# Performance work log

Measured on AMD Instinct MI355X. Metric: run time of the kernel, lower is better.

The kernel has to match this reference:

```python
import jax, jax.numpy as jnp
import numpy as np
import math

D_MODEL = 1024
NUM_HEADS = 16
ALPHA, BETA, K_SCALE, C_THRESHOLD = 0.7, 0.3, 5.0, 0.3
TAU_SCHEDULE = [0.05, 0.05, 0.05, 0.15, 0.25, 0.35, 0.45, 0.55, 0.65, 0.7, 0.75, 0.8]


def setup_inputs() -> dict:
    key = jax.random.key(0)
    ks = jax.random.split(key, 6)
    B, S = 2, 1024
    scale = D_MODEL ** -0.5
    return {
        "x": jax.random.normal(ks[0], (B, S, D_MODEL), dtype=jnp.float32),
        "entropy_prev": jax.random.uniform(ks[1], (B, NUM_HEADS, S, 1), dtype=jnp.float32),
        "Wq": jax.random.normal(ks[2], (D_MODEL, D_MODEL), dtype=jnp.float32) * scale,
        "Wk": jax.random.normal(ks[3], (D_MODEL, D_MODEL), dtype=jnp.float32) * scale,
        "Wv": jax.random.normal(ks[4], (D_MODEL, D_MODEL), dtype=jnp.float32) * scale,
        "Wo": jax.random.normal(ks[5], (D_MODEL, D_MODEL), dtype=jnp.float32) * scale,
        "layer_idx": 4,
    }


def _proj(x, W, B, S, H, Dh):
    # nn.Linear(bias=False): y = x @ W.T ; then [B,S,H,Dh] -> [B,H,S,Dh]
    return jnp.einsum('bsd,ed->bse', x, W).reshape(B, S, H, Dh).transpose(0, 2, 1, 3)


def reference(x, entropy_prev, Wq, Wk, Wv, Wo, layer_idx):
    B, S, _ = x.shape
    H = NUM_HEADS
    Dh = D_MODEL // H
    tau = TAU_SCHEDULE[int(layer_idx)]

    Q = _proj(x, Wq, B, S, H, Dh)
    K = _proj(x, Wk, B, S, H, Dh)
    V = _proj(x, Wv, B, S, H, Dh)

    # raw scores [B,H,S,S]
    scores_raw = jnp.einsum('bhqd,bhkd->bhqk', Q, K) / math.sqrt(Dh)

    # key salience [B,H,1,S]
    sal = jnp.minimum((K * K).sum(axis=-1) / float(Dh), 2.0)
    sal_b = sal[:, :, None, :]

    # WIPER gate [B,H,S,S] (entropy_prev broadcasts over key dim)
    E_t = jax.nn.sigmoid(K_SCALE * (entropy_prev - C_THRESHOLD))
    gate_logit = jnp.clip(E_t * 5.0 + ALPHA * sal_b * 2.0 - BETA * entropy_prev * 1.0, -20.0, 20.0)
    gate = jax.nn.sigmoid(gate_logit)

    mask = gate >= tau
    scores_gated = jnp.where(mask, scores_raw + jnp.log(gate + 1e-8), -jnp.inf)

    best_k_idx = jnp.argmax(scores_raw, axis=-1)  # [B,H,S]
    any_finite = mask.any(axis=-1, keepdims=True)  # [B,H,S,1]

    # safe softmax: degenerate (all -inf) rows replaced by 0s, result discarded below
    attn_raw = jax.nn.softmax(jnp.where(any_finite, scores_gated, 0.0), axis=-1)
    keep_one = jax.nn.one_hot(best_k_idx, S, dtype=x.dtype)
    attn = jnp.where(any_finite, attn_raw, keep_one)

    O = jnp.einsum('bhqk,bhkd->bhqd', attn, V)

    # entropy state: S = log(l) - E[s']
    max_scores = scores_gated.max(axis=-1, keepdims=True)
    shifted = scores_gated - max_scores
    fm = jnp.isfinite(shifted)
    shifted_safe = jnp.where(fm, shifted, 0.0)
    exp_scores = jnp.where(fm, jnp.exp(shifted_safe), 0.0)
    l = jnp.maximum(exp_scores.sum(axis=-1, keepdims=True), 1e-20)
    weighted = (exp_scores * shifted_safe).sum(axis=-1, keepdims=True)
    S_state = jnp.where(any_finite, jnp.log(l) - weighted / l, 0.0)

    out = jnp.einsum('bsd,ed->bse', O.transpose(0, 2, 1, 3).reshape(B, S, D_MODEL), Wo)
    return out, S_state
```

## Files before the change

### kernel.cpp

```cpp
#include <hip/hip_runtime.h>
#include <hip/hip_cooperative_groups.h>
#include <cstdint>

namespace cg = cooperative_groups;

#define DEVINL __device__ __forceinline__

typedef __attribute__((ext_vector_type(8))) short bf16x8;
typedef __attribute__((ext_vector_type(4))) float f32x4;
typedef __attribute__((ext_vector_type(8))) unsigned short u16x8;
typedef unsigned short u16;
typedef unsigned int u32;

#define MFMA16(a, b, c) __builtin_amdgcn_mfma_f32_16x16x32_bf16(a, b, c, 0, 0, 0)

#define LOG2E 1.4426950408889634f
#define LN2 0.69314718055994531f

DEVINL u16 f2bf(float x) {
  u32 u = __builtin_bit_cast(u32, x);
  u += 0x7FFFu + ((u >> 16) & 1u);
  return (u16)(u >> 16);
}
DEVINL float exp2fast(float x) {
  float r;
  asm("v_exp_f32 %0, %1" : "=v"(r) : "v"(x));
  return r;
}
DEVINL void gload_lds16(const void* g, void* l) {
  __builtin_amdgcn_global_load_lds(
      (const __attribute__((address_space(1))) unsigned int*)g,
      (__attribute__((address_space(3))) unsigned int*)l, 16, 0, 0);
}

static constexpr size_t OFF_XB = 0;
static constexpr size_t OFF_WB = 4ull << 20;
static constexpr size_t OFF_Q = 10ull << 20;
static constexpr size_t OFF_K = 14ull << 20;
static constexpr size_t OFF_OB = 18ull << 20;
static constexpr size_t OFF_VT = 22ull << 20;
static constexpr size_t OFF_WOB = 26ull << 20;
static constexpr size_t OFF_FQ = 28ull << 20;
static constexpr size_t OFF_GK = (28ull << 20) + (128ull << 10);

__global__ __launch_bounds__(256, 2) void k_mega(
    const float* __restrict__ x, const float* __restrict__ Wq,
    const float* __restrict__ Wk, const float* __restrict__ Wv,
    const float* __restrict__ Wo, const float* __restrict__ ent,
    char* __restrict__ ws, float* __restrict__ outp) {
  __shared__ __align__(16) char SMEM[81920];
  u16* xb  = (u16*)(ws + OFF_XB);
  u16* Wb  = (u16*)(ws + OFF_WB);
  u16* Qb  = (u16*)(ws + OFF_Q);
  u16* Kb  = (u16*)(ws + OFF_K);
  u16* Ob  = (u16*)(ws + OFF_OB);
  u16* Vtb = (u16*)(ws + OFF_VT);
  u16* Wob = (u16*)(ws + OFF_WOB);
  float* efq = (float*)(ws + OFF_FQ);
  float* egk = (float*)(ws + OFF_GK);
  float* Sst = outp + 2097152;

  cg::grid_group grid = cg::this_grid();
  const int bid = blockIdx.x;
  const int t = threadIdx.x;
  const int lane = t & 63, w = t >> 6;
  const int lm = lane & 15, lg = lane >> 4;

  {
    const int tid = bid * 256 + t;
    for (int g = tid; g < 786432; g += 131072) {
      const float* src; u16* dst; int base;
      if (g < 262144) { src = x; dst = xb; base = g; }
      else {
        int r = (g - 262144) >> 17;
        base = (g - 262144) & 131071;
        src = r == 0 ? Wq : r == 1 ? Wk : r == 2 ? Wv : Wo;
        dst = r == 0 ? Wb : r == 1 ? Wb + 1048576 : r == 2 ? Wb + 2097152 : Wob;
      }
      const float4* s4 = (const float4*)src;
      float4 a = s4[2 * base], b2 = s4[2 * base + 1];
      u16x8 o;
      o[0] = f2bf(a.x);  o[1] = f2bf(a.y);  o[2] = f2bf(a.z);  o[3] = f2bf(a.w);
      o[4] = f2bf(b2.x); o[5] = f2bf(b2.y); o[6] = f2bf(b2.z); o[7] = f2bf(b2.w);
      *(u16x8*)(dst + 8 * base) = o;
    }
    if (bid * 256 + t < 32768) {
      int i = bid * 256 + t;
      float e = ent[i];
      float Et = 1.f / (1.f + __expf(-5.f * (e - 0.3f)));
      efq[i] = __expf(-(5.f * Et - 0.3f * e));
    }
  }
  grid.sync();

  {
    const int wr = w >> 1, wc = w & 1;
    const int rs = t >> 3, cs = t & 7;
    for (int tt = bid; tt < 768; tt += 512) {
      const int m0 = (tt & 31) * 64, n0 = (tt >> 5) * 128;
      f32x4 acc[2][4] = {};
      auto gstage = [&](int buf, int kt) {
        u16* As_ = (u16*)SMEM + buf * 12288;
        u16* Bs_ = As_ + 4096;
#pragma unroll
        for (int i = 0; i < 2; ++i) {
          int rr = rs + 32 * i;
          gload_lds16(xb + (size_t)(m0 + rr) * 1024 + kt + ((cs ^ (rr & 7)) * 8),
                      (char*)As_ + t * 16 + i * 4096);
        }
#pragma unroll
        for (int i = 0; i < 4; ++i) {
          int rr = rs + 32 * i;
          gload_lds16(Wb + (size_t)(n0 + rr) * 1024 + kt + ((cs ^ (rr & 7)) * 8),
                      (char*)Bs_ + t * 16 + i * 4096);
        }
      };
      gstage(0, 0);
      __syncthreads();
      for (int ki = 0; ki < 16; ++ki) {
        const int cur = ki & 1;
        if (ki + 1 < 16) gstage(cur ^ 1, (ki + 1) * 64);
        const u16* As = (u16*)SMEM + cur * 12288;
        const u16* Bs = As + 4096;
#pragma unroll
        for (int ks = 0; ks < 2; ++ks) {
          bf16x8 af[2], bfr[4];
#pragma unroll
          for (int mt = 0; mt < 2; ++mt) {
            int row = wr * 32 + mt * 16 + lm;
            af[mt] = *(const bf16x8*)((const char*)As + row * 128 +
                                      (((ks * 4 + lg) ^ (row & 7)) << 4));
          }
#pragma unroll
          for (int nt = 0; nt < 4; ++nt) {
            int row = wc * 64 + nt * 16 + lm;
            bfr[nt] = *(const bf16x8*)((const char*)Bs + row * 128 +
                                       (((ks * 4 + lg) ^ (row & 7)) << 4));
          }
#pragma unroll
          for (int mt = 0; mt < 2; ++mt)
#pragma unroll
            for (int nt = 0; nt < 4; ++nt)
              acc[mt][nt] = MFMA16(af[mt], bfr[nt], acc[mt][nt]);
        }
        __syncthreads();
      }
      const int region = n0 >> 10;
      const int b = m0 >> 10, s0 = m0 & 1023;
      if (region < 2) {
        u16* dst = region == 0 ? Qb : Kb;
        const float scl = region == 0 ? 0.125f * LOG2E : 1.f;
#pragma unroll
        for (int mt = 0; mt < 2; ++mt)
#pragma unroll
          for (int nt = 0; nt < 4; ++nt)
#pragma unroll
            for (int r = 0; r < 4; ++r) {
              int m = m0 + wr * 32 + mt * 16 + lg * 4 + r;
              int n = n0 + wc * 64 + nt * 16 + lm;
              int e = n & 1023, h = e >> 6, d = e & 63;
              dst[(size_t)(((b << 4) + h) * 1024 + (m & 1023)) * 64 + d] =
                  f2bf(acc[mt][nt][r] * scl);
            }
        if (region == 1) {
          int hh = ((n0 - 1024) >> 6) + wc;
#pragma unroll
          for (int mt = 0; mt < 2; ++mt)
#pragma unroll
            for (int r = 0; r < 4; ++r) {
              float ss = 0.f;
#pragma unroll
              for (int nt = 0; nt < 4; ++nt) ss += acc[mt][nt][r] * acc[mt][nt][r];
              ss += __shfl_xor(ss, 1);
              ss += __shfl_xor(ss, 2);
              ss += __shfl_xor(ss, 4);
              ss += __shfl_xor(ss, 8);
              if (lm == 0) {
                int s = s0 + wr * 32 + mt * 16 + lg * 4 + r;
                float g = 1.4f * fminf(ss * (1.f / 64.f), 2.f);
                egk[(size_t)((b << 4) + hh) * 1024 + s] = __expf(-g);
              }
            }
        }
      } else {
        u16* tile = (u16*)SMEM;
#pragma unroll
        for (int half = 0; half < 2; ++half) {
          if (wc == half) {
#pragma unroll
            for (int mt = 0; mt < 2; ++mt)
#pragma unroll
              for (int nt = 0; nt < 4; ++nt)
#pragma unroll
                for (int r = 0; r < 4; ++r) {
                  int d = nt * 16 + lm;
                  int mloc = wr * 32 + mt * 16 + lg * 4 + r;
                  tile[d * 64 + (mloc ^ ((d & 7) << 3))] = f2bf(acc[mt][nt][r]);
                }
          }
          __syncthreads();
          int hh = ((n0 - 2048) >> 6) + half;
#pragma unroll
          for (int j = 0; j < 2; ++j) {
            int dd = (t >> 3) + 32 * j, mc = t & 7;
            u16x8 v = *(const u16x8*)&tile[dd * 64 + ((mc * 8) ^ ((dd & 7) << 3))];
            *(u16x8*)(Vtb + ((size_t)(((b << 4) + hh) * 64 + dd)) * 1024 + s0 +
                      mc * 8) = v;
          }
          __syncthreads();
        }
      }
    }
  }
  grid.sync();

  {
    const int bh = bid >> 4, qblk = bid & 15;
    const int b = bh >> 4, h = bh & 15;
    const size_t bhS = (size_t)bh << 10;
    const int qb = qblk * 64 + w * 16;
    u16* KsA = (u16*)SMEM;
    u16* VsA = (u16*)(SMEM + 32768);
    u32* PsA = (u32*)(SMEM + 65536);

    auto stage = [&](int buf, int k0) {
      int rowK = t >> 3, cK = t & 7;
      int rowV = t >> 4, cV = t & 15;
#pragma unroll
      for (int i2 = 0; i2 < 4; ++i2) {
        int rr = rowK + 32 * i2;
        gload_lds16(Kb + (bhS + k0 + rr) * 64 + ((cK ^ (rr & 7)) * 8),
                    (char*)(KsA + buf * 8192) + t * 16 + i2 * 4096);
        int dd2 = rowV + 16 * i2;
        gload_lds16(Vtb + ((size_t)bh * 64 + dd2) * 1024 + k0 + ((cV ^ (dd2 & 15)) * 8),
                    (char*)(VsA + buf * 8192) + t * 16 + i2 * 4096);
      }
    };

    bf16x8 qf[2];
#pragma unroll
    for (int ks = 0; ks < 2; ++ks)
      qf[ks] = *(const bf16x8*)(Qb + (bhS + qb + lm) * 64 + ks * 32 + lg * 8);
    const float efql = efq[bhS + qb + lm];

    f32x4 Oacc[4] = {};
    float m_r = -1e30f, l_r = 0.f, W_r = 0.f;

    stage(0, 0);
    f32x4 egN[8];
#pragma unroll
    for (int nt = 0; nt < 8; ++nt)
      egN[nt] = *(const f32x4*)&egk[bhS + nt * 16 + lg * 4];
    __syncthreads();

    for (int kt = 0; kt < 8; ++kt) {
      const int cur = kt & 1;
      if (kt < 7) stage(cur ^ 1, (kt + 1) * 128);

      f32x4 c_[8];
      __builtin_amdgcn_s_setprio(1);
#pragma unroll
      for (int nt = 0; nt < 8; ++nt) {
        c_[nt] = (f32x4){0.f, 0.f, 0.f, 0.f};
#pragma unroll
        for (int ks = 0; ks < 2; ++ks) {
          int row = nt * 16 + lm;
          int byo = (((ks * 4 + lg) ^ (row & 7)) << 4);
          bf16x8 kb = *(const bf16x8*)((const char*)(KsA + cur * 8192) + row * 128 + byo);
          c_[nt] = MFMA16(kb, qf[ks], c_[nt]);
        }
      }
      __builtin_amdgcn_s_setprio(0);

      float v_[8][4];
      float lmax = -3e38f;
#pragma unroll
      for (int nt = 0; nt < 8; ++nt) {
        f32x4 eg = egN[nt];
#pragma unroll
        for (int r = 0; r < 4; ++r) {
          float xg = efql * eg[r];
          v_[nt][r] = c_[nt][r] - __log2f(1.f + xg);
        }
        lmax = fmaxf(fmaxf(lmax, v_[nt][0]),
                     fmaxf(fmaxf(v_[nt][1], v_[nt][2]), v_[nt][3]));
      }
      if (kt < 7) {
#pragma unroll
        for (int nt = 0; nt < 8; ++nt)
          egN[nt] = *(const f32x4*)&egk[bhS + (kt + 1) * 128 + nt * 16 + lg * 4];
      }
      lmax = fmaxf(lmax, __shfl_xor(lmax, 16));
      lmax = fmaxf(lmax, __shfl_xor(lmax, 32));

      if (__any(lmax > m_r + 7.2134752f)) {
        float mn = fmaxf(m_r, lmax);
        float dd = m_r - mn;
        float sc = exp2fast(dd);
        W_r = sc * (W_r + dd * l_r);
        l_r *= sc;
        m_r = mn;
        float scO[4];
#pragma unroll
        for (int r = 0; r < 4; ++r) scO[r] = __shfl(sc, (lane & 48) | (lg * 4 + r));
#pragma unroll
        for (int dt = 0; dt < 4; ++dt)
#pragma unroll
          for (int r = 0; r < 4; ++r) Oacc[dt][r] *= scO[r];
      }

      float psum = 0.f, wsum = 0.f;
      u32 pw[16];
#pragma unroll
      for (int nt = 0; nt < 8; ++nt) {
        float p_[4];
#pragma unroll
        for (int r = 0; r < 4; ++r) {
          float sh = v_[nt][r] - m_r;
          float p = exp2fast(sh);
          p_[r] = p;
          psum += p;
          wsum = fmaf(p, sh, wsum);
        }
        asm("v_cvt_pk_bf16_f32 %0, %1, %2" : "=v"(pw[nt*2+0]) : "v"(p_[0]), "v"(p_[1]));
        asm("v_cvt_pk_bf16_f32 %0, %1, %2" : "=v"(pw[nt*2+1]) : "v"(p_[2]), "v"(p_[3]));
      }
      psum += __shfl_xor(psum, 16);
      psum += __shfl_xor(psum, 32);
      wsum += __shfl_xor(wsum, 16);
      wsum += __shfl_xor(wsum, 32);
      l_r += psum;
      W_r += wsum;

      u32* prow = PsA + (w * 16 + lm) * 64;
      const int sw = (lm & 7) << 2;
#pragma unroll
      for (int nt = 0; nt < 8; ++nt) {
        int idx = (nt * 8 + lg * 2) ^ sw;
        uint2 pr;
        pr.x = pw[nt * 2 + 0];
        pr.y = pw[nt * 2 + 1];
        *(uint2*)(prow + idx) = pr;
      }

      bf16x8 pa[4];
#pragma unroll
      for (int ks = 0; ks < 4; ++ks) {
        int idx = (ks * 16 + lg * 4) ^ sw;
        pa[ks] = *(const bf16x8*)(prow + idx);
      }
      __builtin_amdgcn_s_setprio(1);
#pragma unroll
      for (int dt = 0; dt < 4; ++dt) {
#pragma unroll
        for (int ks = 0; ks < 4; ++ks) {
          int row = dt * 16 + lm;
          int byo = (((ks * 4 + lg) ^ (row & 15)) << 4);
          bf16x8 vb = *(const bf16x8*)((const char*)(VsA + cur * 8192) + row * 256 + byo);
          Oacc[dt] = MFMA16(pa[ks], vb, Oacc[dt]);
        }
      }
      __builtin_amdgcn_s_setprio(0);
      __syncthreads();
    }

    float invl = 1.f / l_r;
    float entv = __logf(l_r) - (W_r * LN2) * invl;
    float invO[4];
#pragma unroll
    for (int r = 0; r < 4; ++r) invO[r] = __shfl(invl, (lane & 48) | (lg * 4 + r));
#pragma unroll
    for (int dt = 0; dt < 4; ++dt)
#pragma unroll
      for (int r = 0; r < 4; ++r) {
        int srow = qb + lg * 4 + r;
        int col = h * 64 + dt * 16 + lm;
        Ob[(size_t)(b * 1024 + srow) * 1024 + col] = f2bf(Oacc[dt][r] * invO[r]);
      }
    if (lg == 0) Sst[bhS + qb + lm] = entv;
  }
  grid.sync();

  {
    const int wr = w >> 1, wc = w & 1;
    const int rs = t >> 3, cs = t & 7;
    const int m0 = (bid & 31) * 64, n0 = (bid >> 5) * 64;
    f32x4 acc[2][2] = {};
    auto gstage = [&](int buf, int kt) {
      u16* As_ = (u16*)SMEM + buf * 8192;
      u16* Bs_ = As_ + 4096;
#pragma unroll
      for (int i = 0; i < 2; ++i) {
        int rr = rs + 32 * i;
        gload_lds16(Ob + (size_t)(m0 + rr) * 1024 + kt + ((cs ^ (rr & 7)) * 8),
                    (char*)As_ + t * 16 + i * 4096);
        gload_lds16(Wob + (size_t)(n0 + rr) * 1024 + kt + ((cs ^ (rr & 7)) * 8),
                    (char*)Bs_ + t * 16 + i * 4096);
      }
    };
    gstage(0, 0);
    __syncthreads();
    for (int ki = 0; ki < 16; ++ki) {
      const int cur = ki & 1;
      if (ki + 1 < 16) gstage(cur ^ 1, (ki + 1) * 64);
      const u16* As = (u16*)SMEM + cur * 8192;
      const u16* Bs = As + 4096;
#pragma unroll
      for (int ks = 0; ks < 2; ++ks) {
        bf16x8 af[2], bfr[2];
#pragma unroll
        for (int mt = 0; mt < 2; ++mt) {
          int row = wr * 32 + mt * 16 + lm;
          af[mt] = *(const bf16x8*)((const char*)As + row * 128 +
                                    (((ks * 4 + lg) ^ (row & 7)) << 4));
        }
#pragma unroll
        for (int nt = 0; nt < 2; ++nt) {
          int row = wc * 32 + nt * 16 + lm;
          bfr[nt] = *(const bf16x8*)((const char*)Bs + row * 128 +
                                     (((ks * 4 + lg) ^ (row & 7)) << 4));
        }
#pragma unroll
        for (int mt = 0; mt < 2; ++mt)
#pragma unroll
          for (int nt = 0; nt < 2; ++nt)
            acc[mt][nt] = MFMA16(af[mt], bfr[nt], acc[mt][nt]);
      }
      __syncthreads();
    }
#pragma unroll
    for (int mt = 0; mt < 2; ++mt)
#pragma unroll
      for (int nt = 0; nt < 2; ++nt)
#pragma unroll
        for (int r = 0; r < 4; ++r) {
          int m = m0 + wr * 32 + mt * 16 + lg * 4 + r;
          int n = n0 + wc * 32 + nt * 16 + lm;
          outp[(size_t)m * 1024 + n] = acc[mt][nt][r];
        }
  }
}

__global__ __launch_bounds__(256) void k_prep(const float* __restrict__ x,
                                              const float* __restrict__ Wq,
                                              const float* __restrict__ Wk,
                                              const float* __restrict__ Wv,
                                              const float* __restrict__ Wo,
                                              const float* __restrict__ ent,
                                              u16* __restrict__ xb,
                                              u16* __restrict__ Wb,
                                              u16* __restrict__ Wob,
                                              float* __restrict__ efq) {
  const int bid = blockIdx.x;
  if (bid < 3072) {
    const float* src;
    u16* dst;
    int base;
    if (bid < 1024)      { src = x;  dst = xb;            base = bid; }
    else if (bid < 1536) { src = Wq; dst = Wb;            base = bid - 1024; }
    else if (bid < 2048) { src = Wk; dst = Wb + (1u<<20); base = bid - 1536; }
    else if (bid < 2560) { src = Wv; dst = Wb + (2u<<20); base = bid - 2048; }
    else                 { src = Wo; dst = Wob;           base = bid - 2560; }
    int i = base * 256 + threadIdx.x;
    const float4* s4 = (const float4*)src;
    float4 a = s4[2 * i], b = s4[2 * i + 1];
    u16x8 o;
    o[0] = f2bf(a.x); o[1] = f2bf(a.y); o[2] = f2bf(a.z); o[3] = f2bf(a.w);
    o[4] = f2bf(b.x); o[5] = f2bf(b.y); o[6] = f2bf(b.z); o[7] = f2bf(b.w);
    *(u16x8*)(dst + 8 * i) = o;
  } else {
    int i = (bid - 3072) * 256 + threadIdx.x;
    float e = ent[i];
    float Et = 1.f / (1.f + __expf(-5.f * (e - 0.3f)));
    efq[i] = __expf(-(5.f * Et - 0.3f * e));
  }
}

template <int BM, int BN, int NDIM, int MODE>
__global__ __launch_bounds__(256) void k_gemm(const u16* __restrict__ A,
                                              const u16* __restrict__ Bw,
                                              int Kdim, u16* __restrict__ Qo,
                                              u16* __restrict__ Ko,
                                              u16* __restrict__ Vt,
                                              float* __restrict__ egk_out,
                                              float* __restrict__ Cout) {
  constexpr int MT = BM / 32, NT = BN / 32;
  constexpr int MB = 2048 / BM, NB = NDIM / BN;
  constexpr int CPX = MB * NB / 8;
  __shared__ __align__(16) u16 SM[2][(BM + BN) * 64];
  const int t = threadIdx.x;
  const int lb = (blockIdx.x & 7) * CPX + (blockIdx.x >> 3);
  const int m0 = (lb % MB) * BM, n0 = (lb / MB) * BN;
  const int lane = t & 63, w = t >> 6;
  const int wr = w >> 1, wc = w & 1, lm = lane & 15, lg = lane >> 4;
  const int rs = t >> 3, cs = t & 7;
  f32x4 acc[MT][NT] = {};
#define GSTAGE(buf, kt)                                                        \
  {                                                                            \
    u16* As_ = SM[buf];                                                        \
    u16* Bs_ = SM[buf] + BM * 64;                                              \
    _Pragma("unroll") for (int i = 0; i < BM / 32; ++i) {                      \
      int rr = rs + 32 * i;                                                    \
      gload_lds16(A + (size_t)(m0 + rr) * Kdim + (kt) + ((cs ^ (rr & 7)) * 8), \
                  (char*)As_ + t * 16 + i * 4096);                             \
    }                                                                          \
    _Pragma("unroll") for (int i = 0; i < BN / 32; ++i) {                      \
      int rr = rs + 32 * i;                                                    \
      gload_lds16(Bw + (size_t)(n0 + rr) * Kdim + (kt) + ((cs ^ (rr & 7)) * 8),\
                  (char*)Bs_ + t * 16 + i * 4096);                             \
    }                                                                          \
  }
  GSTAGE(0, 0);
  __syncthreads();
  const int nk = Kdim >> 6;
  for (int ki = 0; ki < nk; ++ki) {
    const int cur = ki & 1;
    if (ki + 1 < nk) GSTAGE(cur ^ 1, (ki + 1) * 64);
    const u16* As = SM[cur];
    const u16* Bs = SM[cur] + BM * 64;
#pragma unroll
    for (int ks = 0; ks < 2; ++ks) {
      bf16x8 af[MT], bfr[NT];
#pragma unroll
      for (int mt = 0; mt < MT; ++mt) {
        int row = wr * (BM / 2) + mt * 16 + lm;
        af[mt] = *(const bf16x8*)((const char*)As + row * 128 +
                                  (((ks * 4 + lg) ^ (row & 7)) << 4));
      }
#pragma unroll
      for (int nt = 0; nt < NT; ++nt) {
        int row = wc * (BN / 2) + nt * 16 + lm;
        bfr[nt] = *(const bf16x8*)((const char*)Bs + row * 128 +
                                   (((ks * 4 + lg) ^ (row & 7)) << 4));
      }
#pragma unroll
      for (int mt = 0; mt < MT; ++mt)
#pragma unroll
        for (int nt = 0; nt < NT; ++nt)
          acc[mt][nt] = MFMA16(af[mt], bfr[nt], acc[mt][nt]);
    }
    __syncthreads();
  }
#undef GSTAGE
  if (MODE == 1) {
#pragma unroll
    for (int mt = 0; mt < MT; ++mt)
#pragma unroll
      for (int nt = 0; nt < NT; ++nt)
#pragma unroll
        for (int r = 0; r < 4; ++r) {
          int m = m0 + wr * (BM / 2) + mt * 16 + lg * 4 + r;
          int n = n0 + wc * (BN / 2) + nt * 16 + lm;
          Cout[(size_t)m * 1024 + n] = acc[mt][nt][r];
        }
    return;
  }
  const int region = n0 >> 10;
  const int b = m0 >> 10, s0 = m0 & 1023;
  if (region < 2) {
    u16* dst = region == 0 ? Qo : Ko;
    const float scl = region == 0 ? 0.125f * LOG2E : 1.f;
#pragma unroll
    for (int mt = 0; mt < MT; ++mt)
#pragma unroll
      for (int nt = 0; nt < NT; ++nt)
#pragma unroll
        for (int r = 0; r < 4; ++r) {
          int m = m0 + wr * (BM / 2) + mt * 16 + lg * 4 + r;
          int n = n0 + wc * (BN / 2) + nt * 16 + lm;
          int e = n & 1023, h = e >> 6, d = e & 63;
          dst[(size_t)(((b << 4) + h) * 1024 + (m & 1023)) * 64 + d] =
              f2bf(acc[mt][nt][r] * scl);
        }
    if (region == 1) {
      int hh = ((n0 - 1024) >> 6) + wc;
#pragma unroll
      for (int mt = 0; mt < MT; ++mt)
#pragma unroll
        for (int r = 0; r < 4; ++r) {
          float ss = 0.f;
#pragma unroll
          for (int nt = 0; nt < NT; ++nt) ss += acc[mt][nt][r] * acc[mt][nt][r];
          ss += __shfl_xor(ss, 1);
          ss += __shfl_xor(ss, 2);
          ss += __shfl_xor(ss, 4);
          ss += __shfl_xor(ss, 8);
          if (lm == 0) {
            int s = s0 + wr * (BM / 2) + mt * 16 + lg * 4 + r;
            float g = 1.4f * fminf(ss * (1.f / 64.f), 2.f);
            egk_out[(size_t)(((b << 4) + hh)) * 1024 + s] = __expf(-g);
          }
        }
    }
  } else {
    u16* tile = SM[0];
#pragma unroll
    for (int half = 0; half < 2; ++half) {
      if (wc == half) {
#pragma unroll
        for (int mt = 0; mt < MT; ++mt)
#pragma unroll
          for (int nt = 0; nt < NT; ++nt)
#pragma unroll
            for (int r = 0; r < 4; ++r) {
              int d = nt * 16 + lm;
              int mloc = wr * (BM / 2) + mt * 16 + lg * 4 + r;
              tile[d * 64 + (mloc ^ ((d & 7) << 3))] = f2bf(acc[mt][nt][r]);
            }
      }
      __syncthreads();
      int hh = ((n0 - 2048) >> 6) + half;
#pragma unroll
      for (int j = 0; j < 2; ++j) {
        int dd = (t >> 3) + 32 * j, mc = t & 7;
        u16x8 v = *(const u16x8*)&tile[dd * 64 + ((mc * 8) ^ ((dd & 7) << 3))];
        *(u16x8*)(Vt + ((size_t)(((b << 4) + hh) * 64 + dd)) * 1024 + s0 + mc * 8) = v;
      }
      __syncthreads();
    }
  }
}

__global__ __launch_bounds__(256, 2) void k_attn(const u16* __restrict__ Q,
                                                 const u16* __restrict__ Kt,
                                                 const u16* __restrict__ Vt,
                                                 const float* __restrict__ efq,
                                                 const float* __restrict__ egk,
                                                 u16* __restrict__ Ob,
                                                 float* __restrict__ Sst) {
  __shared__ __align__(16) u16 Ks[2][128 * 64];
  __shared__ __align__(16) u16 Vs[2][64 * 128];
  __shared__ __align__(16) u32 Ps[4][16][64];
  const int i = blockIdx.x;
  const int lb = ((i & 7) << 6) | (i >> 3);
  const int bh = lb >> 4, qblk = lb & 15;
  const int t = threadIdx.x, lane = t & 63, w = t >> 6;
  const int lm = lane & 15, lg = lane >> 4;
  const int b = bh >> 4, h = bh & 15;
  const size_t bhS = (size_t)bh << 10;
  const int qb = qblk * 64 + w * 16;
#define STAGE(buf, k0)                                                         \
  {                                                                            \
    int rowK = t >> 3, cK = t & 7;                                             \
    int rowV = t >> 4, cV = t & 15;                                            \
    _Pragma("unroll") for (int i2 = 0; i2 < 4; ++i2) {                         \
      int rr = rowK + 32 * i2;                                                 \
      gload_lds16(Kt + (bhS + (k0) + rr) * 64 + ((cK ^ (rr & 7)) * 8),         \
                  (char*)Ks[buf] + t * 16 + i2 * 4096);                        \
      int dd2 = rowV + 16 * i2;                                                \
      gload_lds16(Vt + ((size_t)bh * 64 + dd2) * 1024 + (k0) +                 \
                      ((cV ^ (dd2 & 15)) * 8),                                 \
                  (char*)Vs[buf] + t * 16 + i2 * 4096);                        \
    }                                                                          \
  }
  bf16x8 qf[2];
#pragma unroll
  for (int ks = 0; ks < 2; ++ks)
    qf[ks] = *(const bf16x8*)(Q + (bhS + qb + lm) * 64 + ks * 32 + lg * 8);
  const float efql = efq[bhS + qb + lm];
  f32x4 Oacc[4] = {};
  float m_r = -1e30f, l_r = 0.f, W_r = 0.f;
  STAGE(0, 0);
  f32x4 egN[8];
#pragma unroll
  for (int nt = 0; nt < 8; ++nt)
    egN[nt] = *(const f32x4*)&egk[bhS + nt * 16 + lg * 4];
  __syncthreads();
  for (int kt = 0; kt < 8; ++kt) {
    const int cur = kt & 1;
    if (kt < 7) STAGE(cur ^ 1, (kt + 1) * 128);
    f32x4 c_[8];
    __builtin_amdgcn_s_setprio(1);
#pragma unroll
    for (int nt = 0; nt < 8; ++nt) {
      c_[nt] = (f32x4){0.f, 0.f, 0.f, 0.f};
#pragma unroll
      for (int ks = 0; ks < 2; ++ks) {
        int row = nt * 16 + lm;
        int byo = (((ks * 4 + lg) ^ (row & 7)) << 4);
        bf16x8 kb = *(const bf16x8*)((const char*)Ks[cur] + row * 128 + byo);
        c_[nt] = MFMA16(kb, qf[ks], c_[nt]);
      }
    }
    __builtin_amdgcn_s_setprio(0);
    float v_[8][4];
    float lmax = -3e38f;
#pragma unroll
    for (int nt = 0; nt < 8; ++nt) {
      f32x4 eg = egN[nt];
#pragma unroll
      for (int r = 0; r < 4; ++r) {
        float xg = efql * eg[r];
        v_[nt][r] = c_[nt][r] - __log2f(1.f + xg);
      }
      lmax = fmaxf(fmaxf(lmax, v_[nt][0]),
                   fmaxf(fmaxf(v_[nt][1], v_[nt][2]), v_[nt][3]));
    }
    if (kt < 7) {
#pragma unroll
      for (int nt = 0; nt < 8; ++nt)
        egN[nt] = *(const f32x4*)&egk[bhS + (kt + 1) * 128 + nt * 16 + lg * 4];
    }
    lmax = fmaxf(lmax, __shfl_xor(lmax, 16));
    lmax = fmaxf(lmax, __shfl_xor(lmax, 32));
    if (__any(lmax > m_r + 7.2134752f)) {
      float mn = fmaxf(m_r, lmax);
      float dd = m_r - mn;
      float sc = exp2fast(dd);
      W_r = sc * (W_r + dd * l_r);
      l_r *= sc;
      m_r = mn;
      float scO[4];
#pragma unroll
      for (int r = 0; r < 4; ++r) scO[r] = __shfl(sc, (lane & 48) | (lg * 4 + r));
#pragma unroll
      for (int dt = 0; dt < 4; ++dt)
#pragma unroll
        for (int r = 0; r < 4; ++r) Oacc[dt][r] *= scO[r];
    }
    float psum = 0.f, wsum = 0.f;
    u32 pw[16];
#pragma unroll
    for (int nt = 0; nt < 8; ++nt) {
      float p_[4];
#pragma unroll
      for (int r = 0; r < 4; ++r) {
        float sh = v_[nt][r] - m_r;
        float p = exp2fast(sh);
        p_[r] = p;
        psum += p;
        wsum = fmaf(p, sh, wsum);
      }
      asm("v_cvt_pk_bf16_f32 %0, %1, %2" : "=v"(pw[nt*2+0]) : "v"(p_[0]), "v"(p_[1]));
      asm("v_cvt_pk_bf16_f32 %0, %1, %2" : "=v"(pw[nt*2+1]) : "v"(p_[2]), "v"(p_[3]));
    }
    psum += __shfl_xor(psum, 16);
    psum += __shfl_xor(psum, 32);
    wsum += __shfl_xor(wsum, 16);
    wsum += __shfl_xor(wsum, 32);
    l_r += psum;
    W_r += wsum;
    u32* prow = &Ps[w][lm][0];
    const int sw = (lm & 7) << 2;
#pragma unroll
    for (int nt = 0; nt < 8; ++nt) {
      int idx = (nt * 8 + lg * 2) ^ sw;
      uint2 pr;
      pr.x = pw[nt * 2 + 0];
      pr.y = pw[nt * 2 + 1];
      *(uint2*)(prow + idx) = pr;
    }
    bf16x8 pa[4];
#pragma unroll
    for (int ks = 0; ks < 4; ++ks) {
      int idx = (ks * 16 + lg * 4) ^ sw;
      pa[ks] = *(const bf16x8*)(prow + idx);
    }
    __builtin_amdgcn_s_setprio(1);
#pragma unroll
    for (int dt = 0; dt < 4; ++dt) {
#pragma unroll
      for (int ks = 0; ks < 4; ++ks) {
        int row = dt * 16 + lm;
        int byo = (((ks * 4 + lg) ^ (row & 15)) << 4);
        bf16x8 vb = *(const bf16x8*)((const char*)Vs[cur] + row * 256 + byo);
        Oacc[dt] = MFMA16(pa[ks], vb, Oacc[dt]);
      }
    }
    __builtin_amdgcn_s_setprio(0);
    __syncthreads();
  }
  float invl = 1.f / l_r;
  float entv = __logf(l_r) - (W_r * LN2) * invl;
  float invO[4];
#pragma unroll
  for (int r = 0; r < 4; ++r) invO[r] = __shfl(invl, (lane & 48) | (lg * 4 + r));
#pragma unroll
  for (int dt = 0; dt < 4; ++dt)
#pragma unroll
    for (int r = 0; r < 4; ++r) {
      int srow = qb + lg * 4 + r;
      int col = h * 64 + dt * 16 + lm;
      Ob[(size_t)(b * 1024 + srow) * 1024 + col] = f2bf(Oacc[dt][r] * invO[r]);
    }
  if (lg == 0) Sst[bhS + qb + lm] = entv;
#undef STAGE
}

extern "C" void kernel_launch(void* const* d_in, const int* in_sizes, int n_in,
                              void* d_out, int out_size, void* d_ws, size_t ws_size,
                              hipStream_t stream) {
  const float* x = (const float*)d_in[0];
  const float* ent = (const float*)d_in[1];
  const float* Wq = (const float*)d_in[2];
  const float* Wk = (const float*)d_in[3];
  const float* Wv = (const float*)d_in[4];
  const float* Wo = (const float*)d_in[5];
  (void)in_sizes; (void)n_in; (void)out_size; (void)ws_size;

  char* ws = (char*)d_ws;
  float* outp = (float*)d_out;

  int occ = 0;
  hipError_t qe = hipOccupancyMaxActiveBlocksPerMultiprocessor(
      &occ, (const void*)k_mega, 256, 0);
  if (qe == hipSuccess && occ >= 2) {
    void* args[8] = {(void*)&x, (void*)&Wq, (void*)&Wk, (void*)&Wv,
                     (void*)&Wo, (void*)&ent, (void*)&ws, (void*)&outp};
    hipLaunchCooperativeKernel((void*)k_mega, dim3(512), dim3(256), args, 0,
                               stream);
    return;
  }

  u16* xb = (u16*)(ws + OFF_XB);
  u16* Wb = (u16*)(ws + OFF_WB);
  u16* Qb = (u16*)(ws + OFF_Q);
  u16* Kb = (u16*)(ws + OFF_K);
  u16* Ob = (u16*)(ws + OFF_OB);
  u16* Vtb = (u16*)(ws + OFF_VT);
  u16* Wob = (u16*)(ws + OFF_WOB);
  float* efqd = (float*)(ws + OFF_FQ);
  float* egkd = (float*)(ws + OFF_GK);
  float* Sst = outp + 2u * 1024u * 1024u;

  k_prep<<<3200, 256, 0, stream>>>(x, Wq, Wk, Wv, Wo, ent, xb, Wb, Wob, efqd);
  k_gemm<64, 128, 3072, 0><<<768, 256, 0, stream>>>(xb, Wb, 1024, Qb, Kb, Vtb,
                                                    egkd, nullptr);
  k_attn<<<512, 256, 0, stream>>>(Qb, Kb, Vtb, efqd, egkd, Ob, Sst);
  k_gemm<64, 64, 1024, 1><<<512, 256, 0, stream>>>(Ob, Wob, 1024, nullptr, nullptr,
                                                   nullptr, nullptr, outp);
}
```

Baseline: 67.47 us.

## Replace grid syncs with per-tile dataflow counters and shrink attention K tiles

Swaps the two grid-wide barriers after the QKV GEMM and after attention for per-(column tile, batch) and per-(batch, query block) atomic counters with spin-waits, so attention and output-projection blocks start once their own inputs are ready. QKV tiles are reordered so a head's Q/K/V columns finish early, and attention blocks are rotated to start on later heads. The attention key tile drops from 128 to 64, halving LDS so occupancy is less limited. It also replaces log2(1+x) with a cubic polynomial and splits the softmax sums across accumulators; the polynomial approximation and the spin-waits add accuracy and deadlock risk.

```diff
diff --git a/kernel.cpp b/kernel.cpp
--- a/kernel.cpp
+++ b/kernel.cpp
@@ -32,6 +32,10 @@
       (const __attribute__((address_space(1))) unsigned int*)g,
       (__attribute__((address_space(3))) unsigned int*)l, 16, 0, 0);
 }
+DEVINL void spinwait(int* p, int target) {
+  while (__hip_atomic_load(p, __ATOMIC_RELAXED, __HIP_MEMORY_SCOPE_AGENT) < target)
+    __builtin_amdgcn_s_sleep(2);
+}
 
 static constexpr size_t OFF_XB = 0;
 static constexpr size_t OFF_WB = 4ull << 20;
@@ -42,13 +46,14 @@
 static constexpr size_t OFF_WOB = 26ull << 20;
 static constexpr size_t OFF_FQ = 28ull << 20;
 static constexpr size_t OFF_GK = (28ull << 20) + (128ull << 10);
-
-__global__ __launch_bounds__(256, 2) void k_mega(
+static constexpr size_t OFF_FLAGS = 30ull << 20;
+
+__global__ __launch_bounds__(256, 2) void k_pipe(
     const float* __restrict__ x, const float* __restrict__ Wq,
     const float* __restrict__ Wk, const float* __restrict__ Wv,
     const float* __restrict__ Wo, const float* __restrict__ ent,
     char* __restrict__ ws, float* __restrict__ outp) {
-  __shared__ __align__(16) char SMEM[81920];
+  __shared__ __align__(16) char SMEM[49152];
   u16* xb  = (u16*)(ws + OFF_XB);
   u16* Wb  = (u16*)(ws + OFF_WB);
   u16* Qb  = (u16*)(ws + OFF_Q);
@@ -58,6 +63,8 @@
   u16* Wob = (u16*)(ws + OFF_WOB);
   float* efq = (float*)(ws + OFF_FQ);
   float* egk = (float*)(ws + OFF_GK);
+  int* g0cnt = (int*)(ws + OFF_FLAGS);
+  int* acnt  = (int*)(ws + OFF_FLAGS) + 48;
   float* Sst = outp + 2097152;
 
   cg::grid_group grid = cg::this_grid();
@@ -84,11 +91,10 @@
       o[4] = f2bf(b2.x); o[5] = f2bf(b2.y); o[6] = f2bf(b2.z); o[7] = f2bf(b2.w);
       *(u16x8*)(dst + 8 * base) = o;
     }
-    if (bid * 256 + t < 32768) {
-      int i = bid * 256 + t;
-      float e = ent[i];
+    if (tid < 32768) {
+      float e = ent[tid];
       float Et = 1.f / (1.f + __expf(-5.f * (e - 0.3f)));
-      efq[i] = __expf(-(5.f * Et - 0.3f * e));
+      efq[tid] = __expf(-(5.f * Et - 0.3f * e));
     }
   }
   grid.sync();
@@ -97,7 +103,8 @@
     const int wr = w >> 1, wc = w & 1;
     const int rs = t >> 3, cs = t & 7;
     for (int tt = bid; tt < 768; tt += 512) {
-      const int m0 = (tt & 31) * 64, n0 = (tt >> 5) * 128;
+      const int n_t = tt % 24, m_t = tt / 24;
+      const int m0 = m_t * 64, n0 = n_t * 128;
       f32x4 acc[2][4] = {};
       auto gstage = [&](int buf, int kt) {
         u16* As_ = (u16*)SMEM + buf * 12288;
@@ -210,30 +217,43 @@
           __syncthreads();
         }
       }
-    }
-  }
-  grid.sync();
+      __threadfence();
+      __syncthreads();
+      if (t == 0)
+        __hip_atomic_fetch_add(&g0cnt[n_t * 2 + b], 1, __ATOMIC_RELEASE,
+                               __HIP_MEMORY_SCOPE_AGENT);
+    }
+  }
 
   {
-    const int bh = bid >> 4, qblk = bid & 15;
+    const int u = (bid + 256) & 511;
+    const int bh = u >> 4, qblk = u & 15;
     const int b = bh >> 4, h = bh & 15;
     const size_t bhS = (size_t)bh << 10;
     const int qb = qblk * 64 + w * 16;
+    const int hn = h >> 1;
+    if (t == 0) {
+      spinwait(&g0cnt[hn * 2 + b], 16);
+      spinwait(&g0cnt[(8 + hn) * 2 + b], 16);
+      spinwait(&g0cnt[(16 + hn) * 2 + b], 16);
+      (void)__hip_atomic_load(&g0cnt[hn * 2 + b], __ATOMIC_ACQUIRE,
+                              __HIP_MEMORY_SCOPE_AGENT);
+    }
+    __syncthreads();
+
     u16* KsA = (u16*)SMEM;
-    u16* VsA = (u16*)(SMEM + 32768);
-    u32* PsA = (u32*)(SMEM + 65536);
+    u16* VsA = (u16*)(SMEM + 16384);
+    u32* PsA = (u32*)(SMEM + 32768);
 
     auto stage = [&](int buf, int k0) {
       int rowK = t >> 3, cK = t & 7;
-      int rowV = t >> 4, cV = t & 15;
-#pragma unroll
-      for (int i2 = 0; i2 < 4; ++i2) {
+#pragma unroll
+      for (int i2 = 0; i2 < 2; ++i2) {
         int rr = rowK + 32 * i2;
         gload_lds16(Kb + (bhS + k0 + rr) * 64 + ((cK ^ (rr & 7)) * 8),
-                    (char*)(KsA + buf * 8192) + t * 16 + i2 * 4096);
-        int dd2 = rowV + 16 * i2;
-        gload_lds16(Vtb + ((size_t)bh * 64 + dd2) * 1024 + k0 + ((cV ^ (dd2 & 15)) * 8),
-                    (char*)(VsA + buf * 8192) + t * 16 + i2 * 4096);
+                    (char*)(KsA + buf * 4096) + t * 16 + i2 * 4096);
+        gload_lds16(Vtb + ((size_t)bh * 64 + rr) * 1024 + k0 + ((cK ^ (rr & 7)) * 8),
+                    (char*)(VsA + buf * 4096) + t * 16 + i2 * 4096);
       }
     };
 
@@ -247,48 +267,50 @@
     float m_r = -1e30f, l_r = 0.f, W_r = 0.f;
 
     stage(0, 0);
-    f32x4 egN[8];
-#pragma unroll
-    for (int nt = 0; nt < 8; ++nt)
+    f32x4 egN[4];
+#pragma unroll
+    for (int nt = 0; nt < 4; ++nt)
       egN[nt] = *(const f32x4*)&egk[bhS + nt * 16 + lg * 4];
     __syncthreads();
 
-    for (int kt = 0; kt < 8; ++kt) {
+    for (int kt = 0; kt < 16; ++kt) {
       const int cur = kt & 1;
-      if (kt < 7) stage(cur ^ 1, (kt + 1) * 128);
-
-      f32x4 c_[8];
+      if (kt < 15) stage(cur ^ 1, (kt + 1) * 64);
+
+      f32x4 c_[4];
       __builtin_amdgcn_s_setprio(1);
 #pragma unroll
-      for (int nt = 0; nt < 8; ++nt) {
+      for (int nt = 0; nt < 4; ++nt) {
         c_[nt] = (f32x4){0.f, 0.f, 0.f, 0.f};
 #pragma unroll
         for (int ks = 0; ks < 2; ++ks) {
           int row = nt * 16 + lm;
           int byo = (((ks * 4 + lg) ^ (row & 7)) << 4);
-          bf16x8 kb = *(const bf16x8*)((const char*)(KsA + cur * 8192) + row * 128 + byo);
+          bf16x8 kb = *(const bf16x8*)((const char*)(KsA + cur * 4096) + row * 128 + byo);
           c_[nt] = MFMA16(kb, qf[ks], c_[nt]);
         }
       }
       __builtin_amdgcn_s_setprio(0);
 
-      float v_[8][4];
+      float v_[4][4];
       float lmax = -3e38f;
 #pragma unroll
-      for (int nt = 0; nt < 8; ++nt) {
+      for (int nt = 0; nt < 4; ++nt) {
         f32x4 eg = egN[nt];
 #pragma unroll
         for (int r = 0; r < 4; ++r) {
           float xg = efql * eg[r];
-          v_[nt][r] = c_[nt][r] - __log2f(1.f + xg);
+          float t3 = fmaf(xg, 0.37f, -0.72134752f);
+          float lp = xg * fmaf(xg, t3, 1.4426950f);
+          v_[nt][r] = c_[nt][r] - lp;
         }
         lmax = fmaxf(fmaxf(lmax, v_[nt][0]),
                      fmaxf(fmaxf(v_[nt][1], v_[nt][2]), v_[nt][3]));
       }
-      if (kt < 7) {
-#pragma unroll
-        for (int nt = 0; nt < 8; ++nt)
-          egN[nt] = *(const f32x4*)&egk[bhS + (kt + 1) * 128 + nt * 16 + lg * 4];
+      if (kt < 15) {
+#pragma unroll
+        for (int nt = 0; nt < 4; ++nt)
+          egN[nt] = *(const f32x4*)&egk[bhS + (kt + 1) * 64 + nt * 16 + lg * 4];
       }
       lmax = fmaxf(lmax, __shfl_xor(lmax, 16));
       lmax = fmaxf(lmax, __shfl_xor(lmax, 32));
@@ -309,22 +331,24 @@
           for (int r = 0; r < 4; ++r) Oacc[dt][r] *= scO[r];
       }
 
-      float psum = 0.f, wsum = 0.f;
-      u32 pw[16];
-#pragma unroll
-      for (int nt = 0; nt < 8; ++nt) {
+      float psumR[4] = {0.f, 0.f, 0.f, 0.f}, wsumR[4] = {0.f, 0.f, 0.f, 0.f};
+      u32 pw[8];
+#pragma unroll
+      for (int nt = 0; nt < 4; ++nt) {
         float p_[4];
 #pragma unroll
         for (int r = 0; r < 4; ++r) {
           float sh = v_[nt][r] - m_r;
           float p = exp2fast(sh);
           p_[r] = p;
-          psum += p;
-          wsum = fmaf(p, sh, wsum);
+          psumR[r] += p;
+          wsumR[r] = fmaf(p, sh, wsumR[r]);
         }
         asm("v_cvt_pk_bf16_f32 %0, %1, %2" : "=v"(pw[nt*2+0]) : "v"(p_[0]), "v"(p_[1]));
         asm("v_cvt_pk_bf16_f32 %0, %1, %2" : "=v"(pw[nt*2+1]) : "v"(p_[2]), "v"(p_[3]));
       }
+      float psum = (psumR[0] + psumR[1]) + (psumR[2] + psumR[3]);
+      float wsum = (wsumR[0] + wsumR[1]) + (wsumR[2] + wsumR[3]);
       psum += __shfl_xor(psum, 16);
       psum += __shfl_xor(psum, 32);
       wsum += __shfl_xor(wsum, 16);
@@ -332,10 +356,10 @@
       l_r += psum;
       W_r += wsum;
 
-      u32* prow = PsA + (w * 16 + lm) * 64;
+      u32* prow = PsA + (w * 16 + lm) * 32;
       const int sw = (lm & 7) << 2;
 #pragma unroll
-      for (int nt = 0; nt < 8; ++nt) {
+      for (int nt = 0; nt < 4; ++nt) {
         int idx = (nt * 8 + lg * 2) ^ sw;
         uint2 pr;
         pr.x = pw[nt * 2 + 0];
@@ -343,9 +367,9 @@
         *(uint2*)(prow + idx) = pr;
       }
 
-      bf16x8 pa[4];
-#pragma unroll
-      for (int ks = 0; ks < 4; ++ks) {
+      bf16x8 pa[2];
+#pragma unroll
+      for (int ks = 0; ks < 2; ++ks) {
         int idx = (ks * 16 + lg * 4) ^ sw;
         pa[ks] = *(const bf16x8*)(prow + idx);
       }
@@ -353,10 +377,10 @@
 #pragma unroll
       for (int dt = 0; dt < 4; ++dt) {
 #pragma unroll
-        for (int ks = 0; ks < 4; ++ks) {
+        for (int ks = 0; ks < 2; ++ks) {
           int row = dt * 16 + lm;
-          int byo = (((ks * 4 + lg) ^ (row & 15)) << 4);
-          bf16x8 vb = *(const bf16x8*)((const char*)(VsA + cur * 8192) + row * 256 + byo);
+          int byo = (((ks * 4 + lg) ^ (row & 7)) << 4);
+          bf16x8 vb = *(const bf16x8*)((const char*)(VsA + cur * 4096) + row * 128 + byo);
           Oacc[dt] = MFMA16(pa[ks], vb, Oacc[dt]);
         }
       }
@@ -378,13 +402,25 @@
         Ob[(size_t)(b * 1024 + srow) * 1024 + col] = f2bf(Oacc[dt][r] * invO[r]);
       }
     if (lg == 0) Sst[bhS + qb + lm] = entv;
-  }
-  grid.sync();
+
+    __threadfence();
+    __syncthreads();
+    if (t == 0)
+      __hip_atomic_fetch_add(&acnt[b * 16 + qblk], 1, __ATOMIC_RELEASE,
+                             __HIP_MEMORY_SCOPE_AGENT);
+  }
 
   {
     const int wr = w >> 1, wc = w & 1;
     const int rs = t >> 3, cs = t & 7;
     const int m0 = (bid & 31) * 64, n0 = (bid >> 5) * 64;
+    const int b = m0 >> 10, qblk = (m0 & 1023) >> 6;
+    if (t == 0) {
+      spinwait(&acnt[b * 16 + qblk], 16);
+      (void)__hip_atomic_load(&acnt[b * 16 + qblk], __ATOMIC_ACQUIRE,
+                              __HIP_MEMORY_SCOPE_AGENT);
+    }
+    __syncthreads();
     f32x4 acc[2][2] = {};
     auto gstage = [&](int buf, int kt) {
       u16* As_ = (u16*)SMEM + buf * 8192;
@@ -691,7 +727,9 @@
 #pragma unroll
       for (int r = 0; r < 4; ++r) {
         float xg = efql * eg[r];
-        v_[nt][r] = c_[nt][r] - __log2f(1.f + xg);
+        float t3 = fmaf(xg, 0.37f, -0.72134752f);
+        float lp = xg * fmaf(xg, t3, 1.4426950f);
+        v_[nt][r] = c_[nt][r] - lp;
       }
       lmax = fmaxf(fmaxf(lmax, v_[nt][0]),
                    fmaxf(fmaxf(v_[nt][1], v_[nt][2]), v_[nt][3]));
@@ -718,7 +756,7 @@
 #pragma unroll
         for (int r = 0; r < 4; ++r) Oacc[dt][r] *= scO[r];
     }
-    float psum = 0.f, wsum = 0.f;
+    float psumR[4] = {0.f, 0.f, 0.f, 0.f}, wsumR[4] = {0.f, 0.f, 0.f, 0.f};
     u32 pw[16];
 #pragma unroll
     for (int nt = 0; nt < 8; ++nt) {
@@ -728,12 +766,14 @@
         float sh = v_[nt][r] - m_r;
         float p = exp2fast(sh);
         p_[r] = p;
-        psum += p;
-        wsum = fmaf(p, sh, wsum);
+        psumR[r] += p;
+        wsumR[r] = fmaf(p, sh, wsumR[r]);
       }
       asm("v_cvt_pk_bf16_f32 %0, %1, %2" : "=v"(pw[nt*2+0]) : "v"(p_[0]), "v"(p_[1]));
       asm("v_cvt_pk_bf16_f32 %0, %1, %2" : "=v"(pw[nt*2+1]) : "v"(p_[2]), "v"(p_[3]));
     }
+    float psum = (psumR[0] + psumR[1]) + (psumR[2] + psumR[3]);
+    float wsum = (wsumR[0] + wsumR[1]) + (wsumR[2] + wsumR[3]);
     psum += __shfl_xor(psum, 16);
     psum += __shfl_xor(psum, 32);
     wsum += __shfl_xor(wsum, 16);
@@ -803,11 +843,12 @@
 
   int occ = 0;
   hipError_t qe = hipOccupancyMaxActiveBlocksPerMultiprocessor(
-      &occ, (const void*)k_mega, 256, 0);
+      &occ, (const void*)k_pipe, 256, 0);
   if (qe == hipSuccess && occ >= 2) {
+    hipMemsetAsync(ws + OFF_FLAGS, 0, 512, stream);
     void* args[8] = {(void*)&x, (void*)&Wq, (void*)&Wk, (void*)&Wv,
                      (void*)&Wo, (void*)&ent, (void*)&ws, (void*)&outp};
-    hipLaunchCooperativeKernel((void*)k_mega, dim3(512), dim3(256), args, 0,
+    hipLaunchCooperativeKernel((void*)k_pipe, dim3(512), dim3(256), args, 0,
                                stream);
     return;
   }
```

Measured after the change: 67.11 us. No clear change (-0.5%).
